# Performance work log

Measured on AMD Instinct MI355X. Metric: run time of the kernel, lower is better.

## Reference

```python
import jax, jax.numpy as jnp
import numpy as np

TEMPERATURE = 0.5
EPS = 1e-20


def setup_inputs() -> dict:
    key = jax.random.key(0)
    ks = jax.random.split(key, 7)
    N, T, S = 16, 64, 1024
    SRC, TGT, D = 512, 512, 64
    return {
        "input": jax.random.normal(ks[0], (N, T, TGT), jnp.float32),
        "memory_bank": jax.random.normal(ks[1], (N, S, SRC), jnp.float32),
        "W_q": jax.random.normal(ks[2], (TGT, D), jnp.float32) / np.sqrt(TGT),
        "W_ctx": jax.random.normal(ks[3], (SRC, D), jnp.float32) / np.sqrt(SRC),
        "v": jax.random.normal(ks[4], (D,), jnp.float32) / np.sqrt(D),
        "W_out": jax.random.normal(ks[5], (SRC + TGT, TGT), jnp.float32) / np.sqrt(SRC + TGT),
        "b_out": jax.random.normal(ks[6], (TGT,), jnp.float32) * 0.01,
    }


def reference(input, memory_bank, W_q, W_ctx, v, W_out, b_out):
    # MLP attention score: v^T tanh(W_q q + W_ctx h)
    wq = jnp.einsum("ntd,de->nte", input, W_q)            # [N,T,D]
    uh = jnp.einsum("nsd,de->nse", memory_bank, W_ctx)    # [N,S,D]
    wquh = jnp.tanh(wq[:, :, None, :] + uh[:, None, :, :])  # [N,T,S,D]
    scores = jnp.einsum("ntsd,d->nts", wquh, v)           # [N,T,S]

    log_alpha = jax.nn.log_softmax(scores, axis=-1)
    alpha = jnp.exp(log_alpha)                            # c_align_vectors

    # deterministic context + output
    context_c = jnp.einsum("nts,nsd->ntd", alpha, memory_bank)
    h_c = jnp.tanh(jnp.concatenate([input, context_c], axis=-1) @ W_out + b_out)

    # gumbel-softmax sample (K = n_samples = 1, forced by view_as in original)
    u = jax.random.uniform(jax.random.key(42), log_alpha.shape, jnp.float32)
    g = -jnp.log(-jnp.log(u + EPS) + EPS)                 # gumbel noise
    y_align = jax.nn.softmax((log_alpha + g) / TEMPERATURE, axis=-1)  # [N,T,S]

    context_y = jnp.einsum("nts,nsd->ntd", y_align, memory_bank)
    h_y = jnp.tanh(jnp.concatenate([input, context_y], axis=-1) @ W_out + b_out)

    return jnp.stack([h_c, h_y], axis=0)  # [2,N,T,tgt_dim]
```

## Files before the change

kernel.cpp:

```cpp
#include <hip/hip_runtime.h>
#include <hip/hip_bf16.h>
#include <stdint.h>

#define DEV __device__ __forceinline__

typedef __attribute__((ext_vector_type(8))) short short8;
typedef __attribute__((ext_vector_type(4))) float f32x4;

#define TWO_LOG2E 2.8853900817779268f

DEV unsigned short f2bf(float f) {
  uint32_t u = __float_as_uint(f);
  u += 0x7FFFu + ((u >> 16) & 1u);
  return (unsigned short)(u >> 16);
}

DEV uint2 pk4(float4 f) {
  union { __hip_bfloat162 h; unsigned u; } a, b;
  a.h = __float22bfloat162_rn(make_float2(f.x, f.y));
  b.h = __float22bfloat162_rn(make_float2(f.z, f.w));
  return make_uint2(a.u, b.u);
}

DEV short8 mk8(uint2 lo, uint2 hi) {
  union { short8 s; uint4 u; } t;
  t.u = make_uint4(lo.x, lo.y, hi.x, hi.y);
  return t.s;
}

DEV uint32_t rotl32(uint32_t x, int r) { return (x << r) | (x >> (32 - r)); }

DEV void threefry_0_42(uint32_t x0, uint32_t x1, uint32_t& o0, uint32_t& o1) {
  const uint32_t ks0 = 0u, ks1 = 42u, ks2 = 0x1BD11BDAu ^ 42u;
  x0 += ks0; x1 += ks1;
#define TFR(r) { x0 += x1; x1 = rotl32(x1, (r)); x1 ^= x0; }
  TFR(13) TFR(15) TFR(26) TFR(6)  x0 += ks1; x1 += ks2 + 1u;
  TFR(17) TFR(29) TFR(16) TFR(24) x0 += ks2; x1 += ks0 + 2u;
  TFR(13) TFR(15) TFR(26) TFR(6)  x0 += ks0; x1 += ks1 + 3u;
  TFR(17) TFR(29) TFR(16) TFR(24) x0 += ks1; x1 += ks2 + 4u;
  TFR(13) TFR(15) TFR(26) TFR(6)  x0 += ks2; x1 += ks0 + 5u;
#undef TFR
  o0 = x0; o1 = x1;
}

DEV float wredmax(float v) {
#pragma unroll
  for (int off = 32; off > 0; off >>= 1) v = fmaxf(v, __shfl_xor(v, off));
  return v;
}
DEV float wredsum(float v) {
#pragma unroll
  for (int off = 32; off > 0; off >>= 1) v += __shfl_xor(v, off);
  return v;
}

__global__ __launch_bounds__(256) void prep_kernel(const float* __restrict__ Wctx,
                                                   const float* __restrict__ Wq,
                                                   const float* __restrict__ Wout,
                                                   const float* __restrict__ input,
                                                   unsigned short* __restrict__ WctxT,
                                                   unsigned short* __restrict__ WoutT,
                                                   unsigned short* __restrict__ inputB,
                                                   float* __restrict__ wq2) {
  const int b = blockIdx.x;
  const int tid = threadIdx.x;
  __shared__ float tile[64][65];
  __shared__ unsigned short As[64][32];
  if (b < 136) {
    const float* src; unsigned short* dst; int R, C, br, bc;
    if (b < 128) { src = Wout; dst = WoutT; R = 1024; C = 512; br = (b & 15) * 64; bc = (b >> 4) * 64; }
    else         { src = Wctx; dst = WctxT; R = 512;  C = 64;  br = (b - 128) * 64; bc = 0; }
    const int lr = tid >> 4, lc4 = (tid & 15) * 4;
#pragma unroll
    for (int i = 0; i < 4; ++i) {
      float4 v = *(const float4*)(src + (long)(br + lr + i * 16) * C + bc + lc4);
      tile[lr + i * 16][lc4 + 0] = v.x;
      tile[lr + i * 16][lc4 + 1] = v.y;
      tile[lr + i * 16][lc4 + 2] = v.z;
      tile[lr + i * 16][lc4 + 3] = v.w;
    }
    __syncthreads();
#pragma unroll
    for (int i = 0; i < 4; ++i) {
      int crow = lr + i * 16;
      ushort4 o;
      o.x = f2bf(tile[lc4 + 0][crow]);
      o.y = f2bf(tile[lc4 + 1][crow]);
      o.z = f2bf(tile[lc4 + 2][crow]);
      o.w = f2bf(tile[lc4 + 3][crow]);
      *(ushort4*)(dst + (long)(bc + crow) * R + br + lc4) = o;
    }
    return;
  }
  if (b < 152) {
    const long base = (long)(b - 136) * 32768;
#pragma unroll
    for (int it = 0; it < 32; ++it) {
      long e = base + (it * 256 + tid) * 4;
      float4 f = *(const float4*)(input + e);
      *(uint2*)(inputB + e) = pk4(f);
    }
    return;
  }
  const int mbase = (b - 152) * 64;
  const int srow = tid >> 2, kc = tid & 3;
  const int scol = ((kc ^ (srow & 3)) * 8);
  const int wave = tid >> 6, lane = tid & 63;
  const int wm = (wave >> 1) * 32, wn = (wave & 1) * 32;
  const int q = lane >> 4, r = lane & 15;
  const int c0 = ((q ^ (r & 3)) * 8);
  const float* ap = input + (long)(mbase + srow) * 512 + kc * 8;
  f32x4 acc[2][2];
#pragma unroll
  for (int i = 0; i < 2; ++i)
#pragma unroll
    for (int j = 0; j < 2; ++j) acc[i][j] = (f32x4){0.f, 0.f, 0.f, 0.f};
  for (int k0 = 0; k0 < 512; k0 += 32) {
    float4 fa0 = *(const float4*)(ap + k0);
    float4 fa1 = *(const float4*)(ap + k0 + 4);
    uint2 p0 = pk4(fa0), p1 = pk4(fa1);
    *(uint4*)&As[srow][scol] = make_uint4(p0.x, p0.y, p1.x, p1.y);
    __syncthreads();
    short8 bfrag[2];
#pragma unroll
    for (int j2 = 0; j2 < 2; ++j2) {
      float bv[8];
#pragma unroll
      for (int j = 0; j < 8; ++j)
        bv[j] = Wq[(long)(k0 + q * 8 + j) * 64 + wn + j2 * 16 + r];
      bfrag[j2] = mk8(pk4(make_float4(bv[0], bv[1], bv[2], bv[3])),
                      pk4(make_float4(bv[4], bv[5], bv[6], bv[7])));
    }
    short8 a0 = *(const short8*)&As[wm + r][c0];
    short8 a1 = *(const short8*)&As[wm + 16 + r][c0];
    acc[0][0] = __builtin_amdgcn_mfma_f32_16x16x32_bf16(a0, bfrag[0], acc[0][0], 0, 0, 0);
    acc[0][1] = __builtin_amdgcn_mfma_f32_16x16x32_bf16(a0, bfrag[1], acc[0][1], 0, 0, 0);
    acc[1][0] = __builtin_amdgcn_mfma_f32_16x16x32_bf16(a1, bfrag[0], acc[1][0], 0, 0, 0);
    acc[1][1] = __builtin_amdgcn_mfma_f32_16x16x32_bf16(a1, bfrag[1], acc[1][1], 0, 0, 0);
    __syncthreads();
  }
#pragma unroll
  for (int i2 = 0; i2 < 2; ++i2)
#pragma unroll
    for (int j2 = 0; j2 < 2; ++j2) {
      int gcol = wn + j2 * 16 + r;
#pragma unroll
      for (int reg = 0; reg < 4; ++reg)
        wq2[(long)(mbase + wm + i2 * 16 + q * 4 + reg) * 64 + gcol] =
            acc[i2][j2][reg] * TWO_LOG2E;
    }
}

__global__ __launch_bounds__(256) void gemm_uh(const float* __restrict__ mb,
                                               const unsigned short* __restrict__ WctxT,
                                               float* __restrict__ uhT) {
  __shared__ unsigned short As[64][32];
  __shared__ unsigned short Bs[64][32];
  const int tid = threadIdx.x;
  const int mbase = blockIdx.x * 64;
  const int srow = tid >> 2, kc = tid & 3;
  const int scol = ((kc ^ (srow & 3)) * 8);
  const int wave = tid >> 6, lane = tid & 63;
  const int wm = (wave >> 1) * 32, wn = (wave & 1) * 32;
  const int q = lane >> 4, r = lane & 15;
  const int c0 = ((q ^ (r & 3)) * 8);
  const float* ap = mb + (long)(mbase + srow) * 512 + kc * 8;
  const unsigned short* bp = WctxT + (long)srow * 512 + kc * 8;
  f32x4 acc[2][2];
#pragma unroll
  for (int i = 0; i < 2; ++i)
#pragma unroll
    for (int j = 0; j < 2; ++j) acc[i][j] = (f32x4){0.f, 0.f, 0.f, 0.f};

  float4 fa0 = *(const float4*)(ap);
  float4 fa1 = *(const float4*)(ap + 4);
  uint4 fb = *(const uint4*)(bp);
  for (int k0 = 0; k0 < 512; k0 += 32) {
    uint2 p0 = pk4(fa0), p1 = pk4(fa1);
    *(uint4*)&As[srow][scol] = make_uint4(p0.x, p0.y, p1.x, p1.y);
    *(uint4*)&Bs[srow][scol] = fb;
    __syncthreads();
    if (k0 + 32 < 512) {
      fa0 = *(const float4*)(ap + k0 + 32);
      fa1 = *(const float4*)(ap + k0 + 36);
      fb = *(const uint4*)(bp + k0 + 32);
    }
    short8 a0 = *(const short8*)&As[wm + r][c0];
    short8 a1 = *(const short8*)&As[wm + 16 + r][c0];
    short8 b0 = *(const short8*)&Bs[wn + r][c0];
    short8 b1 = *(const short8*)&Bs[wn + 16 + r][c0];
    acc[0][0] = __builtin_amdgcn_mfma_f32_16x16x32_bf16(a0, b0, acc[0][0], 0, 0, 0);
    acc[0][1] = __builtin_amdgcn_mfma_f32_16x16x32_bf16(a0, b1, acc[0][1], 0, 0, 0);
    acc[1][0] = __builtin_amdgcn_mfma_f32_16x16x32_bf16(a1, b0, acc[1][0], 0, 0, 0);
    acc[1][1] = __builtin_amdgcn_mfma_f32_16x16x32_bf16(a1, b1, acc[1][1], 0, 0, 0);
    __syncthreads();
  }
#pragma unroll
  for (int i2 = 0; i2 < 2; ++i2)
#pragma unroll
    for (int j2 = 0; j2 < 2; ++j2) {
      int gcol = wn + j2 * 16 + r;
      int m = mbase + wm + i2 * 16 + q * 4;
      int n = m >> 10, s0 = m & 1023;
      float4 o;
      o.x = acc[i2][j2][0] * TWO_LOG2E;
      o.y = acc[i2][j2][1] * TWO_LOG2E;
      o.z = acc[i2][j2][2] * TWO_LOG2E;
      o.w = acc[i2][j2][3] * TWO_LOG2E;
      *(float4*)(uhT + (long)n * 65536 + (long)gcol * 1024 + s0) = o;
    }
}

__global__ __launch_bounds__(256) void scores_tile(const float* __restrict__ uhT,
                                                   const float* __restrict__ wq2,
                                                   const float* __restrict__ v,
                                                   float* __restrict__ sc) {
  __shared__ float uhs[64][68];
  __shared__ float wqs[16][64];
  __shared__ float vs[64];
  const int tid = threadIdx.x;
  const int s0 = blockIdx.x * 64, tb = blockIdx.y * 16, n = blockIdx.z;

  *(float4*)(&wqs[0][0] + tid * 4) =
      *(const float4*)(wq2 + ((long)n * 64 + tb) * 64 + tid * 4);
  if (tid < 64) vs[tid] = v[tid];
  {
    const int dr = tid >> 4, c4 = (tid & 15) * 4;
#pragma unroll
    for (int dk = 0; dk < 4; ++dk) {
      int d = dk * 16 + dr;
      *(float4*)&uhs[d][c4] = *(const float4*)(uhT + (long)n * 65536 + (long)d * 1024 + s0 + c4);
    }
  }
  __syncthreads();

  float sumv = 0.f;
#pragma unroll
  for (int c = 0; c < 64; c += 4) {
    float4 vv = *(const float4*)&vs[c];
    sumv += vv.x + vv.y + vv.z + vv.w;
  }

  const int s = tid & 63, wv = tid >> 6;
  const float* w0 = &wqs[wv * 4 + 0][0];
  const float* w1 = &wqs[wv * 4 + 1][0];
  const float* w2 = &wqs[wv * 4 + 2][0];
  const float* w3 = &wqs[wv * 4 + 3][0];
  float a0 = 0.f, a1 = 0.f, a2 = 0.f, a3 = 0.f;
#pragma unroll 16
  for (int d = 0; d < 64; ++d) {
    float u = uhs[d][s];
    float vd = vs[d];
    a0 = fmaf(vd, __builtin_amdgcn_rcpf(1.f + __builtin_amdgcn_exp2f(u + w0[d])), a0);
    a1 = fmaf(vd, __builtin_amdgcn_rcpf(1.f + __builtin_amdgcn_exp2f(u + w1[d])), a1);
    a2 = fmaf(vd, __builtin_amdgcn_rcpf(1.f + __builtin_amdgcn_exp2f(u + w2[d])), a2);
    a3 = fmaf(vd, __builtin_amdgcn_rcpf(1.f + __builtin_amdgcn_exp2f(u + w3[d])), a3);
  }
  float* scp = sc + ((long)n * 64 + tb + wv * 4) * 1024 + s0 + s;
  scp[0]    = fmaf(-2.f, a0, sumv);
  scp[1024] = fmaf(-2.f, a1, sumv);
  scp[2048] = fmaf(-2.f, a2, sumv);
  scp[3072] = fmaf(-2.f, a3, sumv);
}

__global__ __launch_bounds__(256) void softmax_gumbel(const float* __restrict__ sc,
                                                      unsigned short* __restrict__ alphaB,
                                                      unsigned short* __restrict__ yalB) {
  const int tid = threadIdx.x;
  const int nt = blockIdx.x;
  __shared__ float red[4];
  float4 l4 = *(const float4*)(sc + (long)nt * 1024 + tid * 4);
  float lsc[4] = {l4.x, l4.y, l4.z, l4.w};

  const int wv = tid >> 6, ln = tid & 63;
  float m = fmaxf(fmaxf(lsc[0], lsc[1]), fmaxf(lsc[2], lsc[3]));
  m = wredmax(m);
  if (ln == 0) red[wv] = m;
  __syncthreads();
  m = fmaxf(fmaxf(red[0], red[1]), fmaxf(red[2], red[3]));
  __syncthreads();
  float ss = 0.f;
#pragma unroll
  for (int i = 0; i < 4; ++i) ss += __expf(lsc[i] - m);
  ss = wredsum(ss);
  if (ln == 0) red[wv] = ss;
  __syncthreads();
  ss = red[0] + red[1] + red[2] + red[3];
  const float logl = __logf(ss);
  __syncthreads();

  const uint32_t jbase = (uint32_t)nt * 1024u + (uint32_t)tid * 4u;
  float ys[4];
  float4 av;
#pragma unroll
  for (int i = 0; i < 4; ++i) {
    float la = lsc[i] - m - logl;
    ((float*)&av)[i] = __expf(la);
    uint32_t o0, o1;
    threefry_0_42(0u, jbase + i, o0, o1);
    uint32_t bits = o0 ^ o1;
    float u = __uint_as_float((bits >> 9) | 0x3f800000u) - 1.0f;
    float g = -__logf(-__logf(u + 1e-20f) + 1e-20f);
    ys[i] = (la + g) * 2.0f;
  }
  *(uint2*)(alphaB + (long)nt * 1024 + tid * 4) = pk4(av);

  float m2 = fmaxf(fmaxf(ys[0], ys[1]), fmaxf(ys[2], ys[3]));
  m2 = wredmax(m2);
  if (ln == 0) red[wv] = m2;
  __syncthreads();
  m2 = fmaxf(fmaxf(red[0], red[1]), fmaxf(red[2], red[3]));
  __syncthreads();
  float s2 = 0.f;
  float4 ye;
#pragma unroll
  for (int i = 0; i < 4; ++i) { ((float*)&ye)[i] = __expf(ys[i] - m2); s2 += ((float*)&ye)[i]; }
  s2 = wredsum(s2);
  if (ln == 0) red[wv] = s2;
  __syncthreads();
  s2 = red[0] + red[1] + red[2] + red[3];
  const float rinv = __fdividef(1.f, s2);
  ye.x *= rinv; ye.y *= rinv; ye.z *= rinv; ye.w *= rinv;
  *(uint2*)(yalB + (long)nt * 1024 + tid * 4) = pk4(ye);
}

__global__ __launch_bounds__(256) void gemm_ctx_mfma(const unsigned short* __restrict__ alphaB,
                                                     const unsigned short* __restrict__ yalB,
                                                     const float* __restrict__ mb,
                                                     unsigned short* __restrict__ ctxB) {
  __shared__ unsigned short As[64][32];
  const int tid = threadIdx.x;
  const int vt = blockIdx.x >> 4, n = blockIdx.x & 15;
  const int dbase = blockIdx.y * 32;
  const int srow = tid >> 2, kc = tid & 3;
  const int scol = ((kc ^ (srow & 3)) * 8);
  const int wave = tid >> 6, lane = tid & 63;
  const int wm = (wave >> 1) * 32, wn = (wave & 1) * 16;
  const int q = lane >> 4, r = lane & 15;
  const int c0 = ((q ^ (r & 3)) * 8);
  const unsigned short* AB = (vt == 0 ? alphaB : yalB) + (long)n * 65536;
  const unsigned short* apB = AB + (long)srow * 1024 + kc * 8;
  const float* bcol = mb + (long)n * 524288 + dbase + wn + r;
  f32x4 acc[2];
  acc[0] = (f32x4){0.f, 0.f, 0.f, 0.f};
  acc[1] = (f32x4){0.f, 0.f, 0.f, 0.f};

  uint4 fa = *(const uint4*)(apB);
  float bv[8];
#pragma unroll
  for (int j = 0; j < 8; ++j) bv[j] = bcol[(long)(q * 8 + j) * 512];

  for (int k0 = 0; k0 < 1024; k0 += 32) {
    *(uint4*)&As[srow][scol] = fa;
    __syncthreads();
    float4 blo = make_float4(bv[0], bv[1], bv[2], bv[3]);
    float4 bhi = make_float4(bv[4], bv[5], bv[6], bv[7]);
    short8 b0 = mk8(pk4(blo), pk4(bhi));
    if (k0 + 32 < 1024) {
      fa = *(const uint4*)(apB + k0 + 32);
#pragma unroll
      for (int j = 0; j < 8; ++j) bv[j] = bcol[(long)(k0 + 32 + q * 8 + j) * 512];
    }
    short8 a0 = *(const short8*)&As[wm + r][c0];
    short8 a1 = *(const short8*)&As[wm + 16 + r][c0];
    acc[0] = __builtin_amdgcn_mfma_f32_16x16x32_bf16(a0, b0, acc[0], 0, 0, 0);
    acc[1] = __builtin_amdgcn_mfma_f32_16x16x32_bf16(a1, b0, acc[1], 0, 0, 0);
    __syncthreads();
  }
#pragma unroll
  for (int i2 = 0; i2 < 2; ++i2) {
    int gcol = dbase + wn + r;
#pragma unroll
    for (int reg = 0; reg < 4; ++reg) {
      long grow = (long)vt * 1024 + n * 64 + wm + i2 * 16 + q * 4 + reg;
      ctxB[grow * 512 + gcol] = f2bf(acc[i2][reg]);
    }
  }
}

__global__ __launch_bounds__(256) void gemm_out_mfma(const unsigned short* __restrict__ inputB,
                                                     const unsigned short* __restrict__ ctxB,
                                                     const unsigned short* __restrict__ WoutT,
                                                     const float* __restrict__ bout,
                                                     float* __restrict__ out) {
  __shared__ unsigned short As[64][32];
  __shared__ unsigned short Bs[32][32];
  const int tid = threadIdx.x;
  const int mbase = blockIdx.x * 64, nbase = blockIdx.y * 32;
  const int srow = tid >> 2, kc = tid & 3;
  const int scol = ((kc ^ (srow & 3)) * 8);
  const int wave = tid >> 6, lane = tid & 63;
  const int wm = (wave >> 1) * 32, wn = (wave & 1) * 16;
  const int q = lane >> 4, r = lane & 15;
  const int c0 = ((q ^ (r & 3)) * 8);
  const int vv = mbase >> 10, nt = (mbase + srow) & 1023;
  const unsigned short* ap_lo = inputB + (long)nt * 512 + kc * 8;
  const unsigned short* ap_hi = ctxB + (long)(vv * 1024 + nt) * 512 + kc * 8 - 512;
  const int brow = (tid & 127) >> 2;
  const unsigned short* bp = WoutT + (long)(nbase + brow) * 1024 + kc * 8;
  f32x4 acc[2];
  acc[0] = (f32x4){0.f, 0.f, 0.f, 0.f};
  acc[1] = (f32x4){0.f, 0.f, 0.f, 0.f};

  uint4 fa = *(const uint4*)(ap_lo);
  uint4 fb;
  if (tid < 128) fb = *(const uint4*)(bp);
  for (int k0 = 0; k0 < 1024; k0 += 32) {
    *(uint4*)&As[srow][scol] = fa;
    if (tid < 128) *(uint4*)&Bs[brow][(kc ^ (brow & 3)) * 8] = fb;
    __syncthreads();
    int kn = k0 + 32;
    if (kn < 1024) {
      const unsigned short* apn = (kn < 512) ? ap_lo : ap_hi;
      fa = *(const uint4*)(apn + kn);
      if (tid < 128) fb = *(const uint4*)(bp + kn);
    }
    short8 a0 = *(const short8*)&As[wm + r][c0];
    short8 a1 = *(const short8*)&As[wm + 16 + r][c0];
    short8 b0 = *(const short8*)&Bs[wn + r][c0];
    acc[0] = __builtin_amdgcn_mfma_f32_16x16x32_bf16(a0, b0, acc[0], 0, 0, 0);
    acc[1] = __builtin_amdgcn_mfma_f32_16x16x32_bf16(a1, b0, acc[1], 0, 0, 0);
    __syncthreads();
  }
#pragma unroll
  for (int i2 = 0; i2 < 2; ++i2) {
    int gcol = nbase + wn + r;
    float bb = bout[gcol];
#pragma unroll
    for (int reg = 0; reg < 4; ++reg) {
      int grow = mbase + wm + i2 * 16 + q * 4 + reg;
      float z = acc[i2][reg] + bb;
      float rc = __builtin_amdgcn_rcpf(1.f + __builtin_amdgcn_exp2f(z * TWO_LOG2E));
      out[(long)grow * 512 + gcol] = fmaf(-2.f, rc, 1.f);
    }
  }
}

extern "C" void kernel_launch(void* const* d_in, const int* in_sizes, int n_in,
                              void* d_out, int out_size, void* d_ws, size_t ws_size,
                              hipStream_t stream) {
  const float* input = (const float*)d_in[0];
  const float* mb    = (const float*)d_in[1];
  const float* W_q   = (const float*)d_in[2];
  const float* W_ctx = (const float*)d_in[3];
  const float* v     = (const float*)d_in[4];
  const float* W_out = (const float*)d_in[5];
  const float* b_out = (const float*)d_in[6];
  float* out = (float*)d_out;
  float* ws = (float*)d_ws;

  float* uhT   = ws;
  float* wq2   = ws + 1048576;
  float* sc    = ws + 1114112;
  unsigned short* alphaB = (unsigned short*)(ws + 2162688);
  unsigned short* yalB   = (unsigned short*)(ws + 2686976);
  unsigned short* inputB = (unsigned short*)(ws + 3211264);
  unsigned short* WctxT  = (unsigned short*)(ws + 3473408);
  unsigned short* WoutT  = (unsigned short*)(ws + 3489792);
  unsigned short* ctxB   = (unsigned short*)uhT;

  prep_kernel<<<168, 256, 0, stream>>>(W_ctx, W_q, W_out, input, WctxT, WoutT, inputB, wq2);
  gemm_uh<<<256, 256, 0, stream>>>(mb, WctxT, uhT);
  scores_tile<<<dim3(16, 4, 16), 256, 0, stream>>>(uhT, wq2, v, sc);
  softmax_gumbel<<<1024, 256, 0, stream>>>(sc, alphaB, yalB);
  gemm_ctx_mfma<<<dim3(32, 16), 256, 0, stream>>>(alphaB, yalB, mb, ctxB);
  gemm_out_mfma<<<dim3(32, 16), 256, 0, stream>>>(inputB, ctxB, WoutT, b_out, out);
}
```

Before: 155.5 us.

## Fuse score computation into softmax-gumbel kernel, dropping score buffer

Replaces the separate tiled score kernel and the softmax kernel with one kernel per (n,t) row that computes the MLP attention scores from uhT in registers and then runs the softmax/gumbel step. This removes the intermediate score buffer round trip and one launch. In exchange, each row block rereads the full uhT slice for its batch, so uhT is reused through cache rather than shared memory.

```diff
diff --git a/kernel.cpp b/kernel.cpp
--- a/kernel.cpp
+++ b/kernel.cpp
@@ -211,66 +211,50 @@
     }
 }
 
-__global__ __launch_bounds__(256) void scores_tile(const float* __restrict__ uhT,
-                                                   const float* __restrict__ wq2,
-                                                   const float* __restrict__ v,
-                                                   float* __restrict__ sc) {
-  __shared__ float uhs[64][68];
-  __shared__ float wqs[16][64];
-  __shared__ float vs[64];
-  const int tid = threadIdx.x;
-  const int s0 = blockIdx.x * 64, tb = blockIdx.y * 16, n = blockIdx.z;
-
-  *(float4*)(&wqs[0][0] + tid * 4) =
-      *(const float4*)(wq2 + ((long)n * 64 + tb) * 64 + tid * 4);
-  if (tid < 64) vs[tid] = v[tid];
-  {
-    const int dr = tid >> 4, c4 = (tid & 15) * 4;
-#pragma unroll
-    for (int dk = 0; dk < 4; ++dk) {
-      int d = dk * 16 + dr;
-      *(float4*)&uhs[d][c4] = *(const float4*)(uhT + (long)n * 65536 + (long)d * 1024 + s0 + c4);
-    }
-  }
-  __syncthreads();
-
-  float sumv = 0.f;
-#pragma unroll
-  for (int c = 0; c < 64; c += 4) {
-    float4 vv = *(const float4*)&vs[c];
-    sumv += vv.x + vv.y + vv.z + vv.w;
-  }
-
-  const int s = tid & 63, wv = tid >> 6;
-  const float* w0 = &wqs[wv * 4 + 0][0];
-  const float* w1 = &wqs[wv * 4 + 1][0];
-  const float* w2 = &wqs[wv * 4 + 2][0];
-  const float* w3 = &wqs[wv * 4 + 3][0];
-  float a0 = 0.f, a1 = 0.f, a2 = 0.f, a3 = 0.f;
-#pragma unroll 16
-  for (int d = 0; d < 64; ++d) {
-    float u = uhs[d][s];
-    float vd = vs[d];
-    a0 = fmaf(vd, __builtin_amdgcn_rcpf(1.f + __builtin_amdgcn_exp2f(u + w0[d])), a0);
-    a1 = fmaf(vd, __builtin_amdgcn_rcpf(1.f + __builtin_amdgcn_exp2f(u + w1[d])), a1);
-    a2 = fmaf(vd, __builtin_amdgcn_rcpf(1.f + __builtin_amdgcn_exp2f(u + w2[d])), a2);
-    a3 = fmaf(vd, __builtin_amdgcn_rcpf(1.f + __builtin_amdgcn_exp2f(u + w3[d])), a3);
-  }
-  float* scp = sc + ((long)n * 64 + tb + wv * 4) * 1024 + s0 + s;
-  scp[0]    = fmaf(-2.f, a0, sumv);
-  scp[1024] = fmaf(-2.f, a1, sumv);
-  scp[2048] = fmaf(-2.f, a2, sumv);
-  scp[3072] = fmaf(-2.f, a3, sumv);
-}
-
-__global__ __launch_bounds__(256) void softmax_gumbel(const float* __restrict__ sc,
+__global__ __launch_bounds__(256) void scores_softmax(const float* __restrict__ uhT,
+                                                      const float* __restrict__ wq2,
+                                                      const float* __restrict__ v,
                                                       unsigned short* __restrict__ alphaB,
                                                       unsigned short* __restrict__ yalB) {
   const int tid = threadIdx.x;
   const int nt = blockIdx.x;
+  const int n = nt >> 6;
+  __shared__ float wvs[64];
+  __shared__ float vvs[64];
   __shared__ float red[4];
-  float4 l4 = *(const float4*)(sc + (long)nt * 1024 + tid * 4);
-  float lsc[4] = {l4.x, l4.y, l4.z, l4.w};
+  if (tid < 64) {
+    wvs[tid] = wq2[nt * 64 + tid];
+    vvs[tid] = v[tid];
+  }
+  __syncthreads();
+
+  float sumv = 0.f;
+#pragma unroll
+  for (int d = 0; d < 64; d += 4) {
+    float4 vv = *(const float4*)&vvs[d];
+    sumv += vv.x + vv.y + vv.z + vv.w;
+  }
+
+  const float* un = uhT + (long)n * 65536 + tid * 4;
+  float4 racc = make_float4(0.f, 0.f, 0.f, 0.f);
+  for (int db = 0; db < 64; db += 8) {
+    float4 ub[8];
+#pragma unroll
+    for (int j = 0; j < 8; ++j) ub[j] = *(const float4*)(un + (long)(db + j) * 1024);
+#pragma unroll
+    for (int j = 0; j < 8; ++j) {
+      float w = wvs[db + j], vvj = vvs[db + j];
+      racc.x = fmaf(vvj, __builtin_amdgcn_rcpf(1.f + __builtin_amdgcn_exp2f(ub[j].x + w)), racc.x);
+      racc.y = fmaf(vvj, __builtin_amdgcn_rcpf(1.f + __builtin_amdgcn_exp2f(ub[j].y + w)), racc.y);
+      racc.z = fmaf(vvj, __builtin_amdgcn_rcpf(1.f + __builtin_amdgcn_exp2f(ub[j].z + w)), racc.z);
+      racc.w = fmaf(vvj, __builtin_amdgcn_rcpf(1.f + __builtin_amdgcn_exp2f(ub[j].w + w)), racc.w);
+    }
+  }
+  float lsc[4];
+  lsc[0] = fmaf(-2.f, racc.x, sumv);
+  lsc[1] = fmaf(-2.f, racc.y, sumv);
+  lsc[2] = fmaf(-2.f, racc.z, sumv);
+  lsc[3] = fmaf(-2.f, racc.w, sumv);
 
   const int wv = tid >> 6, ln = tid & 63;
   float m = fmaxf(fmaxf(lsc[0], lsc[1]), fmaxf(lsc[2], lsc[3]));
@@ -451,18 +435,16 @@
 
   float* uhT   = ws;
   float* wq2   = ws + 1048576;
-  float* sc    = ws + 1114112;
-  unsigned short* alphaB = (unsigned short*)(ws + 2162688);
-  unsigned short* yalB   = (unsigned short*)(ws + 2686976);
-  unsigned short* inputB = (unsigned short*)(ws + 3211264);
-  unsigned short* WctxT  = (unsigned short*)(ws + 3473408);
-  unsigned short* WoutT  = (unsigned short*)(ws + 3489792);
+  unsigned short* alphaB = (unsigned short*)(ws + 1114112);
+  unsigned short* yalB   = (unsigned short*)(ws + 1638400);
+  unsigned short* inputB = (unsigned short*)(ws + 2162688);
+  unsigned short* WctxT  = (unsigned short*)(ws + 2424832);
+  unsigned short* WoutT  = (unsigned short*)(ws + 2441216);
   unsigned short* ctxB   = (unsigned short*)uhT;
 
   prep_kernel<<<168, 256, 0, stream>>>(W_ctx, W_q, W_out, input, WctxT, WoutT, inputB, wq2);
   gemm_uh<<<256, 256, 0, stream>>>(mb, WctxT, uhT);
-  scores_tile<<<dim3(16, 4, 16), 256, 0, stream>>>(uhT, wq2, v, sc);
-  softmax_gumbel<<<1024, 256, 0, stream>>>(sc, alphaB, yalB);
+  scores_softmax<<<1024, 256, 0, stream>>>(uhT, wq2, v, alphaB, yalB);
   gemm_ctx_mfma<<<dim3(32, 16), 256, 0, stream>>>(alphaB, yalB, mb, ctxB);
   gemm_out_mfma<<<dim3(32, 16), 256, 0, stream>>>(inputB, ctxB, WoutT, b_out, out);
 }
```

Measured after the change: 154.1 us. About the same (-0.9%).
